# Kernel tuning notes

Measured on AMD Instinct MI355X. Metric: run time of the kernel, lower is better.

## Reference

```python
import jax, jax.numpy as jnp
import numpy as np

D = 1024
B, N = 4, 2048

def setup_inputs() -> dict:
    key = jax.random.key(0)
    ks = jax.random.split(key, 7)
    sc = 1.0 / np.sqrt(D)
    return {
        "x": jax.random.normal(ks[0], (B, N, D), dtype=jnp.float32),
        "wq_w": jax.random.normal(ks[1], (D, D), dtype=jnp.float32) * sc,
        "wq_b": jax.random.normal(ks[2], (D,), dtype=jnp.float32) * 0.01,
        "wk_w": jax.random.normal(ks[3], (D, D), dtype=jnp.float32) * sc,
        "wk_b": jax.random.normal(ks[4], (D,), dtype=jnp.float32) * 0.01,
        "wv_w": jax.random.normal(ks[5], (D, D), dtype=jnp.float32) * sc,
        "wv_b": jax.random.normal(ks[6], (D,), dtype=jnp.float32) * 0.01,
    }

def reference(x, wq_w, wq_b, wk_w, wk_b, wv_w, wv_b):
    # torch Linear: y = x @ W^T + b
    q = x @ wq_w.T + wq_b
    k = x @ wk_w.T + wk_b
    v = x @ wv_w.T + wv_b
    d = q.shape[-1]
    s = jnp.einsum("bid,bjd->bij", q, k) / jnp.sqrt(jnp.float32(d))
    # faithful to original: triu then transpose (zeros, NOT -inf, enter the softmax)
    t = jnp.swapaxes(jnp.triu(s), -2, -1)
    p = jax.nn.softmax(t, axis=-2)
    attn = jnp.swapaxes(jnp.triu(p), -2, -1) @ v
    return attn
```

## Files before the change

kernel.cpp:

```cpp
#include <hip/hip_runtime.h>
#include <hip/hip_fp16.h>
#include <cstdint>

typedef _Float16 half8_t __attribute__((ext_vector_type(8)));
typedef float f32x4 __attribute__((ext_vector_type(4)));

#define D_ 1024
#define B_ 4
#define N_ 2048
#define M_ (B_*N_)
#define NC_ 3072

#define OFF_WCAT  0u
#define OFF_BCAT  6291456u
#define OFF_XB    6303744u
#define OFF_Q     23080960u
#define OFF_K     39858176u
#define OFF_V     56635392u
#define OFF_ZP    73412608u
#define OFF_DEXP  74461184u
#define OFF_SV    74493952u
#define OFF_INVD  75542528u
#define OFF_CD    75575296u

__device__ __forceinline__ void gload_lds16(const void* g, void* l) {
  __builtin_amdgcn_global_load_lds(
      (const __attribute__((address_space(1))) unsigned int*)(uintptr_t)g,
      (__attribute__((address_space(3))) unsigned int*)(uintptr_t)l, 16, 0, 0);
}

__device__ __forceinline__ void stage128x64(const __half* rowbase, char* lds, int tid) {
#pragma unroll
  for (int inst = 0; inst < 4; ++inst) {
    int L  = inst * 4096 + tid * 16;
    int r  = L >> 7;
    int cb = L & 127;
    int cbs = cb ^ ((r & 7) << 4);
    gload_lds16((const char*)rowbase + (size_t)r * (D_ * 2) + cbs, lds + L);
  }
}

__device__ __forceinline__ half8_t ldsfrag(const char* lds, int row, int cbyte) {
  int b = (row << 7) + (cbyte ^ ((row & 7) << 4));
  return *reinterpret_cast<const half8_t*>(lds + b);
}

__device__ __forceinline__ void gemm128_core(const __half* Arow0, const __half* Brow0,
                                             char* As, char* Bs, f32x4 acc[4][4]) {
  const int tid  = threadIdx.x;
  const int lane = tid & 63;
  const int wave = tid >> 6;
  const int wm = wave >> 1, wn = wave & 1;
  for (int kt = 0; kt < 16; ++kt) {
    if (kt) __syncthreads();
    stage128x64(Arow0 + kt * 64, As, tid);
    stage128x64(Brow0 + kt * 64, Bs, tid);
    asm volatile("s_waitcnt vmcnt(0)" ::: "memory");
    __syncthreads();
#pragma unroll
    for (int kk = 0; kk < 2; ++kk) {
      const int cbyte = kk * 64 + (lane >> 4) * 16;
      half8_t a[4], b[4];
#pragma unroll
      for (int mf = 0; mf < 4; ++mf) a[mf] = ldsfrag(As, wm * 64 + mf * 16 + (lane & 15), cbyte);
#pragma unroll
      for (int nf = 0; nf < 4; ++nf) b[nf] = ldsfrag(Bs, wn * 64 + nf * 16 + (lane & 15), cbyte);
#pragma unroll
      for (int mf = 0; mf < 4; ++mf)
#pragma unroll
        for (int nf = 0; nf < 4; ++nf)
          acc[mf][nf] = __builtin_amdgcn_mfma_f32_16x16x32_f16(a[mf], b[nf], acc[mf][nf], 0, 0, 0);
    }
  }
}

__device__ __forceinline__ void calc_soff(int tid, int soff[4]) {
#pragma unroll
  for (int i = 0; i < 4; ++i) {
    int L = i * 8192 + tid * 16;
    int s = L >> 10;
    int w = L & 1023;
    w ^= ((w >> 9) & 1) << 5;
    int r  = (s >> 1) * 16 + (w >> 6);
    int kb = (s & 1) * 64 + (w & 63);
    soff[i] = r * 2048 + kb;
  }
}

#define MFMA_QUAD(QM, QN)                                                     \
  _Pragma("unroll")                                                           \
  for (int ks = 0; ks < 2; ++ks)                                              \
    _Pragma("unroll")                                                         \
    for (int mf = 0; mf < 4; ++mf)                                            \
      _Pragma("unroll")                                                       \
      for (int nf = 0; nf < 2; ++nf)                                          \
        acc[(QM)*4 + mf][(QN)*2 + nf] = __builtin_amdgcn_mfma_f32_16x16x32_f16( \
            a[mf][ks], b[(QN)][nf][ks], acc[(QM)*4 + mf][(QN)*2 + nf], 0, 0, 0);

__device__ __forceinline__ void gemm256_8ph(const char* Ag, const char* Bg,
                                            char* smem, f32x4 acc[8][4]) {
  const int tid  = threadIdx.x;
  const int lane = tid & 63;
  const int wave = tid >> 6;
  const int wm = wave >> 2, wn = wave & 3;

  int soff[4];
  calc_soff(tid, soff);
  const int wlane = (((lane & 15) * 64 + (lane >> 4) * 16)) ^ (((lane >> 3) & 1) << 5);

#pragma unroll
  for (int i = 0; i < 4; ++i) gload_lds16(Ag + soff[i], smem + i * 8192 + tid * 16);
#pragma unroll
  for (int i = 0; i < 4; ++i) gload_lds16(Bg + soff[i], smem + 32768 + i * 8192 + tid * 16);
  asm volatile("s_waitcnt vmcnt(0)" ::: "memory");
  __builtin_amdgcn_s_barrier();

  for (int t = 0; t < 16; ++t) {
    char* A0  = smem + ((t & 1) << 16);
    char* B0  = A0 + 32768;
    char* A1  = smem + (((t + 1) & 1) << 16);
    char* B1s = A1 + 32768;
    const half8_t* ap = (const half8_t*)(A0 + wm * 16384 + wlane);
    const half8_t* bp = (const half8_t*)(B0 + wn * 8192 + wlane);
    const char* Agn = Ag + (t + 1) * 128;
    const char* Bgn = Bg + (t + 1) * 128;
    const bool pre = (t < 15);

    half8_t a[4][2];
    half8_t b[2][2][2];

#pragma unroll
    for (int mf = 0; mf < 4; ++mf)
#pragma unroll
      for (int ks = 0; ks < 2; ++ks)
        a[mf][ks] = ap[(mf * 2 + ks) * 64];
#pragma unroll
    for (int nf = 0; nf < 2; ++nf)
#pragma unroll
      for (int ks = 0; ks < 2; ++ks)
        b[0][nf][ks] = bp[(nf * 2 + ks) * 64];
    if (pre) {
#pragma unroll
      for (int i = 0; i < 4; ++i) gload_lds16(Agn + soff[i], A1 + i * 8192 + tid * 16);
    }
    __builtin_amdgcn_s_barrier();
    asm volatile("s_waitcnt lgkmcnt(0)" ::: "memory");
    __builtin_amdgcn_s_setprio(1);
    MFMA_QUAD(0, 0)
    __builtin_amdgcn_s_setprio(0);
    __builtin_amdgcn_s_barrier();

#pragma unroll
    for (int nf = 0; nf < 2; ++nf)
#pragma unroll
      for (int ks = 0; ks < 2; ++ks)
        b[1][nf][ks] = bp[((2 + nf) * 2 + ks) * 64];
    if (pre) {
#pragma unroll
      for (int i = 0; i < 4; ++i) gload_lds16(Bgn + soff[i], B1s + i * 8192 + tid * 16);
    }
    __builtin_amdgcn_s_barrier();
    asm volatile("s_waitcnt lgkmcnt(0)" ::: "memory");
    __builtin_amdgcn_s_setprio(1);
    MFMA_QUAD(0, 1)
    __builtin_amdgcn_s_setprio(0);
    __builtin_amdgcn_s_barrier();

#pragma unroll
    for (int mf = 0; mf < 4; ++mf)
#pragma unroll
      for (int ks = 0; ks < 2; ++ks)
        a[mf][ks] = ap[((4 + mf) * 2 + ks) * 64];
    __builtin_amdgcn_s_barrier();
    asm volatile("s_waitcnt lgkmcnt(0)" ::: "memory");
    __builtin_amdgcn_s_setprio(1);
    MFMA_QUAD(1, 0)
    __builtin_amdgcn_s_setprio(0);
    __builtin_amdgcn_s_barrier();

    __builtin_amdgcn_s_setprio(1);
    MFMA_QUAD(1, 1)
    __builtin_amdgcn_s_setprio(0);
    if (pre) asm volatile("s_waitcnt vmcnt(0)" ::: "memory");
    __builtin_amdgcn_s_barrier();
  }
}

__global__ __launch_bounds__(256) void k_prep(
    const float* __restrict__ x, const float* __restrict__ wq, const float* __restrict__ wk,
    const float* __restrict__ wv, const float* __restrict__ bq, const float* __restrict__ bk,
    const float* __restrict__ bv, __half* __restrict__ xb, __half* __restrict__ wcat,
    float* __restrict__ bcat, float* __restrict__ Zpart) {
  const int NX4 = (M_ * D_) / 4;
  const int NW4 = (D_ * D_) / 4;
  const int TOT = NX4 + 3 * NW4;
  int tid0 = blockIdx.x * 256 + threadIdx.x;
  int stride = gridDim.x * 256;
  for (int i = tid0; i < TOT; i += stride) {
    float4 f; __half* dst;
    if (i < NX4) {
      f = ((const float4*)x)[i];
      dst = xb + 4 * (size_t)i;
    } else {
      int j = i - NX4; int w = j / NW4; int o = j - w * NW4;
      const float* src = (w == 0) ? wq : (w == 1) ? wk : wv;
      f = ((const float4*)src)[o];
      dst = wcat + (size_t)w * (D_ * D_) + 4 * (size_t)o;
    }
    __half h0 = __float2half(f.x), h1 = __float2half(f.y),
           h2 = __float2half(f.z), h3 = __float2half(f.w);
    ushort4 u = { __half_as_ushort(h0), __half_as_ushort(h1),
                  __half_as_ushort(h2), __half_as_ushort(h3) };
    *((ushort4*)dst) = u;
  }
  if (tid0 < NC_)
    bcat[tid0] = (tid0 < 1024) ? bq[tid0] : (tid0 < 2048) ? bk[tid0 - 1024] : bv[tid0 - 2048];
  for (int i = tid0; i < M_ * 32; i += stride) Zpart[i] = 0.f;
}

__global__ __launch_bounds__(256) void k_qkv(
    const __half* __restrict__ xb, const __half* __restrict__ wcat,
    const float* __restrict__ bcat,
    __half* __restrict__ q, __half* __restrict__ kx, __half* __restrict__ v) {
  __shared__ __align__(16) char smem[32768];
  char* As = smem; char* Bs = smem + 16384;
  int bid = blockIdx.x;
  int bm = bid / 24, bn = bid % 24;
  f32x4 acc[4][4];
#pragma unroll
  for (int i = 0; i < 4; ++i)
#pragma unroll
    for (int j = 0; j < 4; ++j) acc[i][j] = f32x4{0.f, 0.f, 0.f, 0.f};
  gemm128_core(xb + (size_t)bm * 128 * D_, wcat + (size_t)bn * 128 * D_, As, Bs, acc);

  const int lane = threadIdx.x & 63;
  const int wave = threadIdx.x >> 6;
  const int wm = wave >> 1, wn = wave & 1;
  int sel = bn >> 3;
  __half* outp = (sel == 0) ? q : (sel == 1) ? kx : v;
#pragma unroll
  for (int nf = 0; nf < 4; ++nf) {
    int nloc = wn * 64 + nf * 16 + (lane & 15);
    float bias = bcat[bn * 128 + nloc];
    int ncol = (bn & 7) * 128 + nloc;
#pragma unroll
    for (int mf = 0; mf < 4; ++mf) {
#pragma unroll
      for (int r = 0; r < 4; ++r) {
        int m = bm * 128 + wm * 64 + mf * 16 + (lane >> 4) * 4 + r;
        outp[(size_t)m * D_ + ncol] = __float2half(acc[mf][nf][r] + bias);
      }
    }
  }
}

__global__ __launch_bounds__(512, 2) void k_stats256(
    const __half* __restrict__ q, const __half* __restrict__ kx,
    float* __restrict__ Zpart, float* __restrict__ dexp) {
  __shared__ __align__(16) char smem[131072];
  int bid = blockIdx.x;
  int tile = (bid & 7) * 18 + (bid >> 3);
  int b = tile / 36;
  int r = tile % 36;
  int ti = 0;
  while (r >= 8 - ti) { r -= 8 - ti; ++ti; }
  int tj = ti + r;

  f32x4 acc[8][4];
#pragma unroll
  for (int i = 0; i < 8; ++i)
#pragma unroll
    for (int j = 0; j < 4; ++j) acc[i][j] = f32x4{0.f, 0.f, 0.f, 0.f};

  const size_t base = (size_t)b * N_ * D_;
  gemm256_8ph((const char*)(q + base + (size_t)ti * 256 * D_),
              (const char*)(kx + base + (size_t)tj * 256 * D_), smem, acc);

  const int lane = threadIdx.x & 63;
  const int wave = threadIdx.x >> 6;
  const int wm = wave >> 2, wn = wave & 3;
  const bool offd = (tj > ti);
  const float scale = 0.03125f;
  int zr0 = b * N_ + ti * 256;
#pragma unroll
  for (int mf = 0; mf < 8; ++mf) {
#pragma unroll
    for (int rr = 0; rr < 4; ++rr) {
      int il = wm * 128 + mf * 16 + (lane >> 4) * 4 + rr;
      float ssum = 0.f;
#pragma unroll
      for (int nf = 0; nf < 4; ++nf) {
        int jl = wn * 64 + nf * 16 + (lane & 15);
        float e = __expf(acc[mf][nf][rr] * scale);
        bool keep = offd || (jl >= il);
        if (!offd && jl == il) dexp[zr0 + il] = e;
        ssum += keep ? e : 0.f;
      }
      ssum += __shfl_xor(ssum, 1);
      ssum += __shfl_xor(ssum, 2);
      ssum += __shfl_xor(ssum, 4);
      ssum += __shfl_xor(ssum, 8);
      if ((lane & 15) == 0)
        Zpart[(size_t)(zr0 + il) * 32 + tj * 4 + wn] = ssum;
    }
  }
}

__global__ __launch_bounds__(256) void k_mid(
    const __half* __restrict__ v, const float* __restrict__ Zpart,
    const float* __restrict__ dexp, float* __restrict__ Sv,
    float* __restrict__ invD, float* __restrict__ cdiag) {
  int slab = blockIdx.x;
  int b = slab >> 6, c = slab & 63;
  int dg = threadIdx.x;
  int d0 = dg * 4;
  const ushort4* vp = (const ushort4*)(v + ((size_t)(b * N_ + c * 32)) * D_ + d0);
  f32x4 s = {0.f, 0.f, 0.f, 0.f};
#pragma unroll 8
  for (int r2 = 0; r2 < 32; ++r2) {
    ushort4 u = vp[r2 * (D_ / 4)];
    s[0] += __half2float(__ushort_as_half(u.x));
    s[1] += __half2float(__ushort_as_half(u.y));
    s[2] += __half2float(__ushort_as_half(u.z));
    s[3] += __half2float(__ushort_as_half(u.w));
  }
  *(f32x4*)(Sv + (size_t)slab * D_ + d0) = s;

  int tid = blockIdx.x * 256 + threadIdx.x;
  if (tid < M_) {
    const f32x4* zp = (const f32x4*)(Zpart + (size_t)tid * 32);
    f32x4 z4 = {0.f, 0.f, 0.f, 0.f};
#pragma unroll
    for (int t = 0; t < 8; ++t) {
      f32x4 zz = zp[t];
      z4[0] += zz[0]; z4[1] += zz[1]; z4[2] += zz[2]; z4[3] += zz[3];
    }
    float z = z4[0] + z4[1] + z4[2] + z4[3];
    float Dd = (float)(tid & (N_ - 1)) + z;
    float iv = 1.f / Dd;
    invD[tid] = iv;
    cdiag[tid] = dexp[tid] * iv;
  }
}

__global__ __launch_bounds__(256) void k_out(
    const __half* __restrict__ v, const float* __restrict__ Sv,
    const float* __restrict__ invD, const float* __restrict__ cdiag,
    float* __restrict__ out) {
  __shared__ float sInv[32], sCd[32];
  int slab = blockIdx.x;
  int b = slab >> 6, c = slab & 63;
  int dg = threadIdx.x;
  int d0 = dg * 4;
  int zi0 = b * N_ + c * 32;
  if (dg < 32) sInv[dg] = invD[zi0 + dg];
  else if (dg < 64) sCd[dg - 32] = cdiag[zi0 + dg - 32];
  __syncthreads();

  f32x4 run = {0.f, 0.f, 0.f, 0.f};
  for (int cc = 0; cc < c; ++cc) {
    f32x4 sv = *(const f32x4*)(Sv + (size_t)((b << 6) + cc) * D_ + d0);
    run[0] += sv[0]; run[1] += sv[1]; run[2] += sv[2]; run[3] += sv[3];
  }
  const ushort4* vp = (const ushort4*)(v + (size_t)zi0 * D_ + d0);
  float* op = out + (size_t)zi0 * D_ + d0;
#pragma unroll 4
  for (int r2 = 0; r2 < 32; ++r2) {
    ushort4 u = vp[r2 * (D_ / 4)];
    f32x4 vi;
    vi[0] = __half2float(__ushort_as_half(u.x));
    vi[1] = __half2float(__ushort_as_half(u.y));
    vi[2] = __half2float(__ushort_as_half(u.z));
    vi[3] = __half2float(__ushort_as_half(u.w));
    float iv = sInv[r2], cd = sCd[r2];
    f32x4 o;
    o[0] = run[0] * iv + cd * vi[0];
    o[1] = run[1] * iv + cd * vi[1];
    o[2] = run[2] * iv + cd * vi[2];
    o[3] = run[3] * iv + cd * vi[3];
    *(f32x4*)(op + (size_t)r2 * D_) = o;
    run[0] += vi[0]; run[1] += vi[1]; run[2] += vi[2]; run[3] += vi[3];
  }
}

extern "C" void kernel_launch(void* const* d_in, const int* in_sizes, int n_in,
                              void* d_out, int out_size, void* d_ws, size_t ws_size,
                              hipStream_t stream) {
  const float* x  = (const float*)d_in[0];
  const float* wq = (const float*)d_in[1];
  const float* bq = (const float*)d_in[2];
  const float* wk = (const float*)d_in[3];
  const float* bk = (const float*)d_in[4];
  const float* wv = (const float*)d_in[5];
  const float* bv = (const float*)d_in[6];
  float* out = (float*)d_out;
  char* ws = (char*)d_ws;

  __half* wcat = (__half*)(ws + OFF_WCAT);
  float*  bcat = (float*)(ws + OFF_BCAT);
  __half* xb   = (__half*)(ws + OFF_XB);
  __half* q    = (__half*)(ws + OFF_Q);
  __half* k    = (__half*)(ws + OFF_K);
  __half* v    = (__half*)(ws + OFF_V);
  float* Zpart = (float*)(ws + OFF_ZP);
  float* dexp  = (float*)(ws + OFF_DEXP);
  float* Sv    = (float*)(ws + OFF_SV);
  float* invD  = (float*)(ws + OFF_INVD);
  float* cdiag = (float*)(ws + OFF_CD);

  k_prep<<<dim3(2048), dim3(256), 0, stream>>>(x, wq, wk, wv, bq, bk, bv, xb, wcat, bcat, Zpart);
  k_qkv<<<dim3(64 * 24), dim3(256), 0, stream>>>(xb, wcat, bcat, q, k, v);
  k_stats256<<<dim3(144), dim3(512), 0, stream>>>(q, k, Zpart, dexp);
  k_mid<<<dim3(256), dim3(256), 0, stream>>>(v, Zpart, dexp, Sv, invD, cdiag);
  k_out<<<dim3(256), dim3(256), 0, stream>>>(v, Sv, invD, cdiag, out);
}
```

Baseline: 136.8 us.

## Fuse V column sums into QKV epilogue and drop the middle kernel

Per-32-row slab sums of V (Sv) are now computed in the QKV GEMM epilogue from fp32 accumulators using warp shuffles, removing the separate k_mid pass that re-read V. The Zpart reduction and inverse denominator are moved into k_out, which sums only the valid tile partials, so Zpart no longer needs zero-initialisation in k_prep. This saves one launch, a V read and the Zpart memset, at the cost of extra epilogue work in the V tiles and a serial per-row reduction in k_out. Sv is now summed from unrounded fp32 values rather than fp16 V, which slightly changes numerics.

```diff
diff --git a/kernel.cpp b/kernel.cpp
--- a/kernel.cpp
+++ b/kernel.cpp
@@ -20,8 +20,6 @@
 #define OFF_ZP    73412608u
 #define OFF_DEXP  74461184u
 #define OFF_SV    74493952u
-#define OFF_INVD  75542528u
-#define OFF_CD    75575296u
 
 __device__ __forceinline__ void gload_lds16(const void* g, void* l) {
   __builtin_amdgcn_global_load_lds(
@@ -190,7 +188,7 @@
     const float* __restrict__ x, const float* __restrict__ wq, const float* __restrict__ wk,
     const float* __restrict__ wv, const float* __restrict__ bq, const float* __restrict__ bk,
     const float* __restrict__ bv, __half* __restrict__ xb, __half* __restrict__ wcat,
-    float* __restrict__ bcat, float* __restrict__ Zpart) {
+    float* __restrict__ bcat) {
   const int NX4 = (M_ * D_) / 4;
   const int NW4 = (D_ * D_) / 4;
   const int TOT = NX4 + 3 * NW4;
@@ -215,13 +213,13 @@
   }
   if (tid0 < NC_)
     bcat[tid0] = (tid0 < 1024) ? bq[tid0] : (tid0 < 2048) ? bk[tid0 - 1024] : bv[tid0 - 2048];
-  for (int i = tid0; i < M_ * 32; i += stride) Zpart[i] = 0.f;
 }
 
 __global__ __launch_bounds__(256) void k_qkv(
     const __half* __restrict__ xb, const __half* __restrict__ wcat,
     const float* __restrict__ bcat,
-    __half* __restrict__ q, __half* __restrict__ kx, __half* __restrict__ v) {
+    __half* __restrict__ q, __half* __restrict__ kx, __half* __restrict__ v,
+    float* __restrict__ Sv) {
   __shared__ __align__(16) char smem[32768];
   char* As = smem; char* Bs = smem + 16384;
   int bid = blockIdx.x;
@@ -249,6 +247,25 @@
       for (int r = 0; r < 4; ++r) {
         int m = bm * 128 + wm * 64 + mf * 16 + (lane >> 4) * 4 + r;
         outp[(size_t)m * D_ + ncol] = __float2half(acc[mf][nf][r] + bias);
+      }
+    }
+    if (sel == 2) {
+      int bloc  = bm >> 4;
+      int cbase = (bm & 15) * 4;
+#pragma unroll
+      for (int chl = 0; chl < 2; ++chl) {
+        float s = 8.f * bias;
+#pragma unroll
+        for (int mf2 = 0; mf2 < 2; ++mf2)
+#pragma unroll
+          for (int r = 0; r < 4; ++r)
+            s += acc[chl * 2 + mf2][nf][r];
+        s += __shfl_xor(s, 16);
+        s += __shfl_xor(s, 32);
+        if ((lane >> 4) == 0) {
+          int ch = wm * 2 + chl;
+          Sv[(size_t)((bloc << 6) + cbase + ch) * D_ + ncol] = s;
+        }
       }
     }
   }
@@ -306,46 +323,9 @@
   }
 }
 
-__global__ __launch_bounds__(256) void k_mid(
-    const __half* __restrict__ v, const float* __restrict__ Zpart,
-    const float* __restrict__ dexp, float* __restrict__ Sv,
-    float* __restrict__ invD, float* __restrict__ cdiag) {
-  int slab = blockIdx.x;
-  int b = slab >> 6, c = slab & 63;
-  int dg = threadIdx.x;
-  int d0 = dg * 4;
-  const ushort4* vp = (const ushort4*)(v + ((size_t)(b * N_ + c * 32)) * D_ + d0);
-  f32x4 s = {0.f, 0.f, 0.f, 0.f};
-#pragma unroll 8
-  for (int r2 = 0; r2 < 32; ++r2) {
-    ushort4 u = vp[r2 * (D_ / 4)];
-    s[0] += __half2float(__ushort_as_half(u.x));
-    s[1] += __half2float(__ushort_as_half(u.y));
-    s[2] += __half2float(__ushort_as_half(u.z));
-    s[3] += __half2float(__ushort_as_half(u.w));
-  }
-  *(f32x4*)(Sv + (size_t)slab * D_ + d0) = s;
-
-  int tid = blockIdx.x * 256 + threadIdx.x;
-  if (tid < M_) {
-    const f32x4* zp = (const f32x4*)(Zpart + (size_t)tid * 32);
-    f32x4 z4 = {0.f, 0.f, 0.f, 0.f};
-#pragma unroll
-    for (int t = 0; t < 8; ++t) {
-      f32x4 zz = zp[t];
-      z4[0] += zz[0]; z4[1] += zz[1]; z4[2] += zz[2]; z4[3] += zz[3];
-    }
-    float z = z4[0] + z4[1] + z4[2] + z4[3];
-    float Dd = (float)(tid & (N_ - 1)) + z;
-    float iv = 1.f / Dd;
-    invD[tid] = iv;
-    cdiag[tid] = dexp[tid] * iv;
-  }
-}
-
 __global__ __launch_bounds__(256) void k_out(
     const __half* __restrict__ v, const float* __restrict__ Sv,
-    const float* __restrict__ invD, const float* __restrict__ cdiag,
+    const float* __restrict__ Zpart, const float* __restrict__ dexp,
     float* __restrict__ out) {
   __shared__ float sInv[32], sCd[32];
   int slab = blockIdx.x;
@@ -353,8 +333,17 @@
   int dg = threadIdx.x;
   int d0 = dg * 4;
   int zi0 = b * N_ + c * 32;
-  if (dg < 32) sInv[dg] = invD[zi0 + dg];
-  else if (dg < 64) sCd[dg - 32] = cdiag[zi0 + dg - 32];
+
+  if (dg < 32) {
+    int i  = c * 32 + dg;
+    int row = zi0 + dg;
+    int t0 = (i >> 8) * 4;
+    float z = 0.f;
+    for (int t = t0; t < 32; ++t) z += Zpart[(size_t)row * 32 + t];
+    float iv = 1.f / ((float)i + z);
+    sInv[dg] = iv;
+    sCd[dg]  = dexp[row] * iv;
+  }
   __syncthreads();
 
   f32x4 run = {0.f, 0.f, 0.f, 0.f};
@@ -405,12 +394,9 @@
   float* Zpart = (float*)(ws + OFF_ZP);
   float* dexp  = (float*)(ws + OFF_DEXP);
   float* Sv    = (float*)(ws + OFF_SV);
-  float* invD  = (float*)(ws + OFF_INVD);
-  float* cdiag = (float*)(ws + OFF_CD);
-
-  k_prep<<<dim3(2048), dim3(256), 0, stream>>>(x, wq, wk, wv, bq, bk, bv, xb, wcat, bcat, Zpart);
-  k_qkv<<<dim3(64 * 24), dim3(256), 0, stream>>>(xb, wcat, bcat, q, k, v);
+
+  k_prep<<<dim3(2048), dim3(256), 0, stream>>>(x, wq, wk, wv, bq, bk, bv, xb, wcat, bcat);
+  k_qkv<<<dim3(64 * 24), dim3(256), 0, stream>>>(xb, wcat, bcat, q, k, v, Sv);
   k_stats256<<<dim3(144), dim3(512), 0, stream>>>(q, k, Zpart, dexp);
-  k_mid<<<dim3(256), dim3(256), 0, stream>>>(v, Zpart, dexp, Sv, invD, cdiag);
-  k_out<<<dim3(256), dim3(256), 0, stream>>>(v, Sv, invD, cdiag, out);
-}
+  k_out<<<dim3(256), dim3(256), 0, stream>>>(v, Sv, Zpart, dexp, out);
+}
```

Result: faster. 133.7 us (-2.3%).
